# Performance work log

Measured on AMD Instinct MI355X. Metric: run time of the kernel, lower is better.

## Reference

```python
import jax, jax.numpy as jnp
import numpy as np

P = 16; IMG = 800; GRID = IMG // P; NP = GRID * GRID  # 2500 patches
D = P * P * 3  # 768
H = 8; HD = D // H; FF = 2048; L = 2; B = 2
NM = NP // 2; NV = NP - NM  # 1250 / 1250


def _ln(x, g, b):
    m = x.mean(-1, keepdims=True)
    v = ((x - m) ** 2).mean(-1, keepdims=True)
    return (x - m) * jax.lax.rsqrt(v + 1e-5) * g + b


def _block(x, qkv_w, qkv_b, out_w, out_b, w1, b1, w2, b2, g1, be1, g2, be2):
    # pre-LN-free MAE block: attn -> add&norm -> FFN -> add&norm (dropout in eval = identity)
    Bb, N, _ = x.shape
    qkv = (x @ qkv_w + qkv_b).reshape(Bb, N, 3, H, HD)
    q, k, v = qkv[:, :, 0], qkv[:, :, 1], qkv[:, :, 2]  # [B,N,H,HD]
    scores = jnp.einsum('bnhd,bmhd->bhnm', q, k) / np.float32(np.sqrt(HD))
    w = jax.nn.softmax(scores, axis=-1)
    ao = jnp.einsum('bhnm,bmhd->bnhd', w, v).reshape(Bb, N, D) @ out_w + out_b
    x = _ln(x + ao, g1, be1)
    f = jax.nn.relu(x @ w1 + b1) @ w2 + b2
    return _ln(x + f, g2, be2)


def _patchify(x):
    Bb = x.shape[0]
    # torch unfold(2,P,P).unfold(3,P,P) -> [B,C,h,w,p,p] -> [B,h*w,C*p*p]
    return x.reshape(Bb, 3, GRID, P, GRID, P).transpose(0, 2, 4, 1, 3, 5).reshape(Bb, NP, D)


def setup_inputs() -> dict:
    key = jax.random.key(0)
    ks = jax.random.split(key, 32)
    inp = {}
    inp['x'] = jax.random.normal(ks[0], (B, 3, IMG, IMG), jnp.float32)
    perm = jax.vmap(lambda k: jax.random.permutation(k, NP))(jax.random.split(ks[1], B))
    inp['visible_idx'] = perm[:, NM:].astype(jnp.int32)  # perm order, like torch
    inp['masked_idx'] = perm[:, :NM].astype(jnp.int32)
    c = [2]
    def nx(shape, s=0.02):
        k = ks[c[0]]; c[0] += 1
        return jax.random.normal(k, shape, jnp.float32) * s
    for p in ['enc', 'dec']:
        inp[p + '_qkv_w'] = nx((L, D, 3 * D)); inp[p + '_qkv_b'] = jnp.zeros((L, 3 * D), jnp.float32)
        inp[p + '_out_w'] = nx((L, D, D));     inp[p + '_out_b'] = jnp.zeros((L, D), jnp.float32)
        inp[p + '_w1'] = nx((L, D, FF));       inp[p + '_b1'] = jnp.zeros((L, FF), jnp.float32)
        inp[p + '_w2'] = nx((L, FF, D));       inp[p + '_b2'] = jnp.zeros((L, D), jnp.float32)
        inp[p + '_g1'] = jnp.ones((L, D), jnp.float32);  inp[p + '_be1'] = jnp.zeros((L, D), jnp.float32)
        inp[p + '_g2'] = jnp.ones((L, D), jnp.float32);  inp[p + '_be2'] = jnp.zeros((L, D), jnp.float32)
    inp['out_w'] = nx((D, D)); inp['out_b'] = jnp.zeros((D,), jnp.float32)
    inp['mask_token'] = nx((D,))
    inp['enc_pos'] = nx((NV, D))
    inp['dec_pos'] = nx((NP, D))
    return inp


def reference(x, visible_idx, masked_idx,
              enc_qkv_w, enc_qkv_b, enc_out_w, enc_out_b, enc_w1, enc_b1, enc_w2, enc_b2,
              enc_g1, enc_be1, enc_g2, enc_be2,
              dec_qkv_w, dec_qkv_b, dec_out_w, dec_out_b, dec_w1, dec_b1, dec_w2, dec_b2,
              dec_g1, dec_be1, dec_g2, dec_be2,
              out_w, out_b, mask_token, enc_pos, dec_pos):
    patches = _patchify(x)                                    # [B,NP,D]
    b_ix = jnp.arange(B)[:, None]
    vis = patches[b_ix, visible_idx]                          # [B,NV,D] in perm order
    h = vis + enc_pos[None]
    for i in range(L):
        h = _block(h, enc_qkv_w[i], enc_qkv_b[i], enc_out_w[i], enc_out_b[i],
                   enc_w1[i], enc_b1[i], enc_w2[i], enc_b2[i],
                   enc_g1[i], enc_be1[i], enc_g2[i], enc_be2[i])
    # torch: full_sequence[mask==0] = visible_patches (row-major positions <- perm-order rows)
    vis_pos = jnp.sort(visible_idx, axis=1)
    full = jnp.broadcast_to(mask_token, (B, NP, D))           # masked positions = mask_token
    full = full.at[b_ix, vis_pos].set(h)
    h = full + dec_pos[None]
    for i in range(L):
        h = _block(h, dec_qkv_w[i], dec_qkv_b[i], dec_out_w[i], dec_out_b[i],
                   dec_w1[i], dec_b1[i], dec_w2[i], dec_b2[i],
                   dec_g1[i], dec_be1[i], dec_g2[i], dec_be2[i])
    return h @ out_w + out_b                                  # [B,NP,D]
```

## Files before the change

kernel.cpp:

```cpp
#include <hip/hip_runtime.h>
#include <hip/hip_bf16.h>
#include <cstdint>
#include <cstddef>


#define NBATCH  2
#define NPATCH  2500
#define NVIS    1250
#define DMODEL  768
#define NHEAD   8
#define HDIM    96
#define FFDIM   2048
#define NPADV   2560

typedef __attribute__((ext_vector_type(8))) short bf16x8;
typedef __attribute__((ext_vector_type(4))) float f32x4;

__device__ __forceinline__ short f2bf(float f){
  union { float f; unsigned u; } x; x.f = f;
  unsigned r = x.u + 0x7fffu + ((x.u >> 16) & 1u);
  return (short)(r >> 16);
}

__device__ __forceinline__ void async_copy16(void* lds, const void* g){
  __builtin_amdgcn_global_load_lds(
      (const __attribute__((address_space(1))) unsigned int*)g,
      (__attribute__((address_space(3))) unsigned int*)lds, 16, 0, 0);
}

struct TJob { const float* src; short* dst; int K; int N; int tile_base; int tiles_x; };
struct TJobs { TJob j[17]; };

__global__ __launch_bounds__(256) void transpose_all_kernel(TJobs jobs){
  int bid = blockIdx.x;
  int ji = 0;
  #pragma unroll
  for (int k=1;k<17;k++) if (bid >= jobs.j[k].tile_base) ji = k;
  TJob jb = jobs.j[ji];
  int lt = bid - jb.tile_base;
  int tx = lt % jb.tiles_x, ty = lt / jb.tiles_x;
  __shared__ float tile[32][33];
  int lx = threadIdx.x & 31, ly = threadIdx.x >> 5;
  #pragma unroll
  for (int r=0;r<4;r++)
    tile[ly + r*8][lx] = jb.src[(size_t)(ty*32 + ly + r*8)*jb.N + tx*32 + lx];
  __syncthreads();
  #pragma unroll
  for (int r=0;r<4;r++)
    jb.dst[(size_t)(tx*32 + ly + r*8)*jb.K + ty*32 + lx] = f2bf(tile[lx][ly + r*8]);
}

template<int MODE>
__global__ __launch_bounds__(256) void gemm_kernel(const short* __restrict__ A,
    const short* __restrict__ Wt, const float* __restrict__ bias,
    short* __restrict__ Cb, float* __restrict__ Cf, int M, int Nc, int K){
  __shared__ short ldsA[128*64];
  __shared__ short ldsB[128*64];
  const int t = threadIdx.x, w = t>>6, ln = t&63;
  const int m0 = blockIdx.x*128, n0 = blockIdx.y*128;
  const int wr = (w>>1)*64, wc = (w&1)*64;
  const f32x4 fz = {0.f,0.f,0.f,0.f};
  f32x4 acc[4][4];
  #pragma unroll
  for (int mi=0;mi<4;mi++)
    #pragma unroll
    for (int ni=0;ni<4;ni++) acc[mi][ni] = fz;
  const int nkt = K >> 6;
  for (int kt=0; kt<nkt; kt++){
    #pragma unroll
    for (int c=0;c<4;c++){
      int chunk = c*256 + t;
      int row = chunk>>3, seg = chunk&7, sgs = seg ^ (row&7);
      int gm = m0 + row; if (gm >= M) gm = M-1;
      async_copy16((char*)ldsA + c*4096 + w*1024, A  + (size_t)gm*K      + kt*64 + sgs*8);
      async_copy16((char*)ldsB + c*4096 + w*1024, Wt + (size_t)(n0+row)*K + kt*64 + sgs*8);
    }
    __syncthreads();
    #pragma unroll
    for (int ks=0;ks<2;ks++){
      bf16x8 af[4], bfr[4];
      #pragma unroll
      for (int mi=0;mi<4;mi++){
        int r = wr + mi*16 + (ln&15);
        int d = ks*4 + (ln>>4);
        af[mi]  = *(const bf16x8*)((const char*)ldsA + r*128 + ((d^(r&7))*16));
        int cc = wc + mi*16 + (ln&15);
        bfr[mi] = *(const bf16x8*)((const char*)ldsB + cc*128 + ((d^(cc&7))*16));
      }
      #pragma unroll
      for (int mi=0;mi<4;mi++)
        #pragma unroll
        for (int ni=0;ni<4;ni++)
          acc[mi][ni] = __builtin_amdgcn_mfma_f32_16x16x32_bf16(af[mi], bfr[ni], acc[mi][ni], 0,0,0);
    }
    __syncthreads();
  }
  float bv[4];
  #pragma unroll
  for (int ni=0;ni<4;ni++) bv[ni] = bias[n0 + wc + ni*16 + (ln&15)];
  #pragma unroll
  for (int mi=0;mi<4;mi++){
    #pragma unroll
    for (int j=0;j<4;j++){
      int gr = m0 + wr + mi*16 + (ln>>4)*4 + j;
      if (gr < M){
        #pragma unroll
        for (int ni=0;ni<4;ni++){
          float v = acc[mi][ni][j] + bv[ni];
          if (MODE==2) v = fmaxf(v, 0.f);
          int gc = n0 + wc + ni*16 + (ln&15);
          if (MODE==1) Cf[(size_t)gr*Nc + gc] = v;
          else         Cb[(size_t)gr*Nc + gc] = f2bf(v);
        }
      }
    }
  }
}

__global__ __launch_bounds__(256) void vtrans_kernel(const short* __restrict__ qkv,
    short* __restrict__ vt, int N){
  int bh = blockIdx.z;
  int b = bh >> 3, h = bh & 7;
  int n0 = blockIdx.x*32, hd0 = blockIdx.y*32;
  __shared__ short tile[32][33];
  int lx = threadIdx.x & 31, ly = threadIdx.x >> 5;
  #pragma unroll
  for (int r=0;r<4;r++){
    int n = n0 + ly + r*8;
    short val = 0;
    if (n < N) val = qkv[(size_t)(b*N+n)*2304 + 1536 + h*96 + hd0 + lx];
    tile[ly+r*8][lx] = val;
  }
  __syncthreads();
  #pragma unroll
  for (int r=0;r<4;r++){
    int hd = hd0 + ly + r*8, n = n0 + lx;
    vt[(size_t)(bh*96 + hd)*NPADV + n] = tile[lx][ly+r*8];
  }
}

__global__ __launch_bounds__(256) void attn_kernel(const short* __restrict__ qkv,
    const short* __restrict__ vt, short* __restrict__ ao, int N, int NT){
  __shared__ short Ks[64*128];
  __shared__ short Vs[96*64];
  __shared__ short Ps[4*1024];
  const int t = threadIdx.x, w = t>>6, ln = t&63;
  const int col = ln & 15, hi = ln >> 4;
  const int bh = blockIdx.y, b = bh >> 3, h = bh & 7;
  const int q0 = blockIdx.x * 64;
  short* Pw = &Ps[w*1024];
  const float scale2 = 0.14724974f;

  bf16x8 qf[3];
  {
    int gq = q0 + w*16 + col; if (gq >= N) gq = N-1;
    const short* qrow = qkv + (size_t)(b*N+gq)*2304 + h*96;
    #pragma unroll
    for (int ks=0;ks<3;ks++)
      qf[ks] = *(const bf16x8*)(qrow + ks*32 + hi*8);
  }
  const f32x4 fz = {0.f,0.f,0.f,0.f};
  f32x4 o[6];
  #pragma unroll
  for (int g=0; g<6; g++) o[g] = fz;
  float mrun = -3e38f;
  float srun = 0.f;

  for (int kt=0; kt<NT; kt++){
    int n0 = kt*64;
    #pragma unroll
    for (int i=0;i<4;i++){
      int chunk = i*256 + t, row = chunk>>4, seg = chunk&15;
      int s2 = seg ^ (row&7);
      int gn = n0 + row; if (gn >= N) gn = N-1;
      const short* src = qkv + (size_t)(b*N+gn)*2304 + 768 + h*96
                       + ((s2 < 12) ? s2*8 : 0);
      async_copy16((char*)Ks + i*4096 + w*1024, src);
    }
    #pragma unroll
    for (int i=0;i<3;i++){
      int chunk = i*256 + t, row = chunk>>3, seg = chunk&7;
      int s2 = seg ^ (row&7);
      const short* src = vt + (size_t)(bh*96 + row)*NPADV + n0 + s2*8;
      async_copy16((char*)Vs + i*4096 + w*1024, src);
    }
    __syncthreads();

    f32x4 s[4];
    __builtin_amdgcn_s_setprio(1);
    #pragma unroll
    for (int tt=0;tt<4;tt++){
      f32x4 sc = fz;
      #pragma unroll
      for (int ks=0;ks<3;ks++){
        int r = tt*16 + col, d = ks*4 + hi;
        bf16x8 kb = *(const bf16x8*)((const char*)Ks + r*256 + ((d ^ (r&7))*16));
        sc = __builtin_amdgcn_mfma_f32_16x16x32_bf16(kb, qf[ks], sc, 0,0,0);
      }
      s[tt] = sc;
    }
    __builtin_amdgcn_s_setprio(0);

    if (n0 + 64 > N){
      #pragma unroll
      for (int tt=0;tt<4;tt++)
        #pragma unroll
        for (int j=0;j<4;j++)
          if (n0 + tt*16 + hi*4 + j >= N) s[tt][j] = -3e38f;
    }
    float mraw = s[0][0];
    #pragma unroll
    for (int tt=0;tt<4;tt++)
      #pragma unroll
      for (int j=0;j<4;j++) if (tt|j) mraw = fmaxf(mraw, s[tt][j]);
    mraw = fmaxf(mraw, __shfl_xor(mraw, 16));
    mraw = fmaxf(mraw, __shfl_xor(mraw, 32));
    float mxs = mraw * scale2;
    if (__any(mxs > mrun + 11.5f)){
      float mnew = fmaxf(mrun, mxs);
      float alpha = exp2f(mrun - mnew);
      mrun = mnew; srun *= alpha;
      float a0 = __shfl(alpha, hi*4+0), a1 = __shfl(alpha, hi*4+1);
      float a2 = __shfl(alpha, hi*4+2), a3 = __shfl(alpha, hi*4+3);
      #pragma unroll
      for (int g=0; g<6; g++){
        o[g][0] *= a0; o[g][1] *= a1; o[g][2] *= a2; o[g][3] *= a3;
      }
    }
    float psum = 0.f;
    #pragma unroll
    for (int tt=0;tt<4;tt++){
      float p0 = exp2f(fmaf(s[tt][0], scale2, -mrun));
      float p1 = exp2f(fmaf(s[tt][1], scale2, -mrun));
      float p2 = exp2f(fmaf(s[tt][2], scale2, -mrun));
      float p3 = exp2f(fmaf(s[tt][3], scale2, -mrun));
      psum += (p0+p1) + (p2+p3);
      __hip_bfloat162 lo = __float22bfloat162_rn(float2{p0,p1});
      __hip_bfloat162 hn = __float22bfloat162_rn(float2{p2,p3});
      uint2 pk; pk.x = *reinterpret_cast<unsigned*>(&lo);
      pk.y = *reinterpret_cast<unsigned*>(&hn);
      char* wp = (char*)Pw + col*128 + (((2*tt + (hi>>1)) ^ (col&7))<<4) + ((hi&1)<<3);
      *reinterpret_cast<uint2*>(wp) = pk;
    }
    srun += psum;
    __builtin_amdgcn_s_setprio(1);
    #pragma unroll
    for (int ks2=0; ks2<2; ks2++){
      bf16x8 pa = *(const bf16x8*)((const char*)Pw + col*128
                    + (((ks2*4 + hi) ^ (col&7))<<4));
      #pragma unroll
      for (int g=0; g<6; g++){
        int r = g*16 + col, d = ks2*4 + hi;
        bf16x8 vb = *(const bf16x8*)((const char*)Vs + r*128 + ((d ^ (r&7))*16));
        o[g] = __builtin_amdgcn_mfma_f32_16x16x32_bf16(pa, vb, o[g], 0,0,0);
      }
    }
    __builtin_amdgcn_s_setprio(0);
    __syncthreads();
  }
  srun += __shfl_xor(srun, 16);
  srun += __shfl_xor(srun, 32);
  float inv = 1.f / srun;
  float i0 = __shfl(inv, hi*4+0), i1 = __shfl(inv, hi*4+1);
  float i2 = __shfl(inv, hi*4+2), i3 = __shfl(inv, hi*4+3);
  #pragma unroll
  for (int g=0; g<6; g++){
    float ov[4] = {o[g][0]*i0, o[g][1]*i1, o[g][2]*i2, o[g][3]*i3};
    #pragma unroll
    for (int j=0;j<4;j++){
      int qr = q0 + w*16 + hi*4 + j;
      if (qr < N)
        ao[(size_t)(b*N+qr)*768 + h*96 + g*16 + col] = f2bf(ov[j]);
    }
  }
}

__global__ __launch_bounds__(256) void ln_kernel(const float* __restrict__ xin,
    const float* __restrict__ add, const float* __restrict__ g,
    const float* __restrict__ be, float* __restrict__ xo, short* __restrict__ xob){
  int row = blockIdx.x, t = threadIdx.x;
  float e[3]; float s = 0.f;
  #pragma unroll
  for (int k=0;k<3;k++){
    size_t off = (size_t)row*768 + t + k*256;
    e[k] = xin[off] + add[off]; s += e[k];
  }
  #pragma unroll
  for (int d=32; d; d>>=1) s += __shfl_xor(s, d);
  __shared__ float red[8];
  if ((t&63)==0) red[t>>6] = s;
  __syncthreads();
  float mean = (red[0]+red[1]+red[2]+red[3]) * (1.f/768.f);
  float vs = 0.f;
  #pragma unroll
  for (int k=0;k<3;k++){ float dd = e[k]-mean; vs += dd*dd; }
  #pragma unroll
  for (int d=32; d; d>>=1) vs += __shfl_xor(vs, d);
  if ((t&63)==0) red[4 + (t>>6)] = vs;
  __syncthreads();
  float rstd = rsqrtf((red[4]+red[5]+red[6]+red[7]) * (1.f/768.f) + 1e-5f);
  #pragma unroll
  for (int k=0;k<3;k++){
    int c = t + k*256;
    size_t off = (size_t)row*768 + c;
    float ov = (e[k]-mean)*rstd*g[c] + be[c];
    xo[off] = ov; xob[off] = f2bf(ov);
  }
}

__global__ __launch_bounds__(256) void patchify_kernel(const float* __restrict__ x,
    const int* __restrict__ vis, const float* __restrict__ enc_pos,
    float* __restrict__ xe, short* __restrict__ xeb){
  int b = blockIdx.y, i = blockIdx.x;
  int pidx = vis[b*NVIS + i];
  int gy = pidx / 50, gx = pidx - gy*50;
  #pragma unroll
  for (int k=0;k<3;k++){
    int d = threadIdx.x + k*256;
    int c = d >> 8, rr = d & 255, py = rr >> 4, px = rr & 15;
    float v = x[(((size_t)b*3 + c)*800 + gy*16 + py)*800 + gx*16 + px]
            + enc_pos[(size_t)i*768 + d];
    size_t off = (size_t)(b*NVIS + i)*768 + d;
    xe[off] = v; xeb[off] = f2bf(v);
  }
}

__global__ __launch_bounds__(256) void rank_kernel(const int* __restrict__ vis,
    int* __restrict__ rnk){
  int b = blockIdx.y; int i = blockIdx.x*256 + threadIdx.x;
  if (i >= NVIS) return;
  int p = vis[b*NVIS + i]; int c = 0;
  for (int j=0;j<NVIS;j++) c += (vis[b*NVIS + j] < p) ? 1 : 0;
  rnk[b*NVIS + i] = c;
}

__global__ __launch_bounds__(256) void dec_init_kernel(const float* __restrict__ mask_token,
    const float* __restrict__ dec_pos, float* __restrict__ xd, short* __restrict__ xdb){
  int row = blockIdx.x;
  int p = row % NPATCH;
  #pragma unroll
  for (int k=0;k<3;k++){
    int c = threadIdx.x + k*256;
    float v = mask_token[c] + dec_pos[(size_t)p*768 + c];
    size_t off = (size_t)row*768 + c;
    xd[off] = v; xdb[off] = f2bf(v);
  }
}

__global__ __launch_bounds__(256) void scatter_kernel(const int* __restrict__ vis,
    const int* __restrict__ rnk, const float* __restrict__ xe,
    const float* __restrict__ dec_pos, float* __restrict__ xd, short* __restrict__ xdb){
  int b = blockIdx.y, i = blockIdx.x;
  int p = vis[b*NVIS+i]; int r = rnk[b*NVIS+i];
  #pragma unroll
  for (int k=0;k<3;k++){
    int c = threadIdx.x + k*256;
    float v = xe[(size_t)(b*NVIS + r)*768 + c] + dec_pos[(size_t)p*768 + c];
    size_t off = (size_t)(b*NPATCH + p)*768 + c;
    xd[off] = v; xdb[off] = f2bf(v);
  }
}

static void run_block(hipStream_t stream, float* xf, short* xb, int M, int N, int NT,
                      const short* wqkvT, const float* qkv_b, const short* woutT,
                      const float* out_b, const short* w1T, const float* b1,
                      const short* w2T, const float* b2,
                      const float* g1, const float* be1, const float* g2, const float* be2,
                      short* qkvb, short* vt, short* aob, short* ffnb, float* tmp){
  int mt = (M + 127)/128;
  gemm_kernel<0><<<dim3(mt, 18), 256, 0, stream>>>(xb, wqkvT, qkv_b, qkvb, nullptr, M, 2304, 768);
  vtrans_kernel<<<dim3(NT*2, 3, 16), 256, 0, stream>>>(qkvb, vt, N);
  attn_kernel<<<dim3(NT, 16), 256, 0, stream>>>(qkvb, vt, aob, N, NT);
  gemm_kernel<1><<<dim3(mt, 6), 256, 0, stream>>>(aob, woutT, out_b, nullptr, tmp, M, 768, 768);
  ln_kernel<<<M, 256, 0, stream>>>(xf, tmp, g1, be1, xf, xb);
  gemm_kernel<2><<<dim3(mt, 16), 256, 0, stream>>>(xb, w1T, b1, ffnb, nullptr, M, 2048, 768);
  gemm_kernel<1><<<dim3(mt, 6), 256, 0, stream>>>(ffnb, w2T, b2, nullptr, tmp, M, 768, 2048);
  ln_kernel<<<M, 256, 0, stream>>>(xf, tmp, g2, be2, xf, xb);
}

extern "C" void kernel_launch(void* const* d_in, const int* in_sizes, int n_in,
                              void* d_out, int out_size, void* d_ws, size_t ws_size,
                              hipStream_t stream){
  const float* x        = (const float*)d_in[0];
  const int*   vis      = (const int*)d_in[1];
  const float* eqkv_w   = (const float*)d_in[3];
  const float* eqkv_b   = (const float*)d_in[4];
  const float* eout_w   = (const float*)d_in[5];
  const float* eout_b   = (const float*)d_in[6];
  const float* ew1      = (const float*)d_in[7];
  const float* eb1      = (const float*)d_in[8];
  const float* ew2      = (const float*)d_in[9];
  const float* eb2      = (const float*)d_in[10];
  const float* eg1      = (const float*)d_in[11];
  const float* ebe1     = (const float*)d_in[12];
  const float* eg2      = (const float*)d_in[13];
  const float* ebe2     = (const float*)d_in[14];
  const float* dqkv_w   = (const float*)d_in[15];
  const float* dqkv_b   = (const float*)d_in[16];
  const float* dout_w   = (const float*)d_in[17];
  const float* dout_b   = (const float*)d_in[18];
  const float* dw1      = (const float*)d_in[19];
  const float* db1      = (const float*)d_in[20];
  const float* dw2      = (const float*)d_in[21];
  const float* db2      = (const float*)d_in[22];
  const float* dg1      = (const float*)d_in[23];
  const float* dbe1     = (const float*)d_in[24];
  const float* dg2      = (const float*)d_in[25];
  const float* dbe2     = (const float*)d_in[26];
  const float* fout_w   = (const float*)d_in[27];
  const float* fout_b   = (const float*)d_in[28];
  const float* mask_tok = (const float*)d_in[29];
  const float* enc_posp = (const float*)d_in[30];
  const float* dec_posp = (const float*)d_in[31];

  char* p = (char*)d_ws;
  auto alloc = [&](size_t bytes)->char*{ char* r = p; p += (bytes + 255) & ~(size_t)255; return r; };

  const float* qkvw_s[2] = {eqkv_w, dqkv_w};
  const float* outw_s[2] = {eout_w, dout_w};
  const float* w1_s[2]   = {ew1, dw1};
  const float* w2_s[2]   = {ew2, dw2};

  short *wq[2][2], *wo[2][2], *w1t[2][2], *w2t[2][2];
  TJobs jobs; int jidx = 0; int tbase = 0;
  auto addJob = [&](const float* src, short* dst, int K, int N){
    jobs.j[jidx].src = src; jobs.j[jidx].dst = dst; jobs.j[jidx].K = K; jobs.j[jidx].N = N;
    jobs.j[jidx].tile_base = tbase; jobs.j[jidx].tiles_x = N/32;
    tbase += (K/32)*(N/32); jidx++;
  };
  for (int s=0;s<2;s++)
    for (int i=0;i<2;i++){
      wq[s][i]  = (short*)alloc((size_t)2304*768*2);
      addJob(qkvw_s[s] + (size_t)i*768*2304, wq[s][i], 768, 2304);
      wo[s][i]  = (short*)alloc((size_t)768*768*2);
      addJob(outw_s[s] + (size_t)i*768*768, wo[s][i], 768, 768);
      w1t[s][i] = (short*)alloc((size_t)2048*768*2);
      addJob(w1_s[s] + (size_t)i*768*2048, w1t[s][i], 768, 2048);
      w2t[s][i] = (short*)alloc((size_t)768*2048*2);
      addJob(w2_s[s] + (size_t)i*2048*768, w2t[s][i], 2048, 768);
    }
  short* wfin = (short*)alloc((size_t)768*768*2);
  addJob(fout_w, wfin, 768, 768);
  int total_tiles = tbase;

  float* xe   = (float*)alloc((size_t)2500*768*4);
  short* xeb  = (short*)alloc((size_t)2500*768*2);
  float* xd   = (float*)alloc((size_t)5000*768*4);
  short* xdb  = (short*)alloc((size_t)5000*768*2);
  short* qkvb = (short*)alloc((size_t)5000*2304*2);
  short* vt   = (short*)alloc((size_t)16*96*NPADV*2);
  short* aob  = (short*)alloc((size_t)5000*768*2);
  short* ffnb = (short*)alloc((size_t)5000*2048*2);
  float* tmp  = (float*)alloc((size_t)5000*768*4);
  int*   rnk  = (int*)alloc((size_t)2*NVIS*4);

  transpose_all_kernel<<<total_tiles, 256, 0, stream>>>(jobs);
  patchify_kernel<<<dim3(NVIS, NBATCH), 256, 0, stream>>>(x, vis, enc_posp, xe, xeb);
  rank_kernel<<<dim3((NVIS+255)/256, NBATCH), 256, 0, stream>>>(vis, rnk);

  for (int i=0;i<2;i++)
    run_block(stream, xe, xeb, 2500, 1250, 20,
              wq[0][i], eqkv_b + i*2304, wo[0][i], eout_b + i*768,
              w1t[0][i], eb1 + i*2048, w2t[0][i], eb2 + i*768,
              eg1 + i*768, ebe1 + i*768, eg2 + i*768, ebe2 + i*768,
              qkvb, vt, aob, ffnb, tmp);

  dec_init_kernel<<<NBATCH*NPATCH, 256, 0, stream>>>(mask_tok, dec_posp, xd, xdb);
  scatter_kernel<<<dim3(NVIS, NBATCH), 256, 0, stream>>>(vis, rnk, xe, dec_posp, xd, xdb);

  for (int i=0;i<2;i++)
    run_block(stream, xd, xdb, 5000, 2500, 40,
              wq[1][i], dqkv_b + i*2304, wo[1][i], dout_b + i*768,
              w1t[1][i], db1 + i*2048, w2t[1][i], db2 + i*768,
              dg1 + i*768, dbe1 + i*768, dg2 + i*768, dbe2 + i*768,
              qkvb, vt, aob, ffnb, tmp);

  gemm_kernel<1><<<dim3(40, 6), 256, 0, stream>>>(xdb, wfin, fout_b, nullptr,
                                                  (float*)d_out, 5000, 768, 768);
}
```

Measured before the change: 1.022 ms.

## Split KV range in attention and split-K the narrow-output GEMMs

```diff
diff --git a/kernel.cpp b/kernel.cpp
--- a/kernel.cpp
+++ b/kernel.cpp
@@ -53,11 +53,13 @@
 template<int MODE>
 __global__ __launch_bounds__(256) void gemm_kernel(const short* __restrict__ A,
     const short* __restrict__ Wt, const float* __restrict__ bias,
-    short* __restrict__ Cb, float* __restrict__ Cf, int M, int Nc, int K){
+    short* __restrict__ Cb, float* __restrict__ Cf0, float* __restrict__ Cf1,
+    int M, int Nc, int K, int nkt_per){
   __shared__ short ldsA[128*64];
   __shared__ short ldsB[128*64];
   const int t = threadIdx.x, w = t>>6, ln = t&63;
   const int m0 = blockIdx.x*128, n0 = blockIdx.y*128;
+  const int z = blockIdx.z;
   const int wr = (w>>1)*64, wc = (w&1)*64;
   const f32x4 fz = {0.f,0.f,0.f,0.f};
   f32x4 acc[4][4];
@@ -65,8 +67,9 @@
   for (int mi=0;mi<4;mi++)
     #pragma unroll
     for (int ni=0;ni<4;ni++) acc[mi][ni] = fz;
-  const int nkt = K >> 6;
-  for (int kt=0; kt<nkt; kt++){
+  const int ktb = z*nkt_per;
+  for (int kk=0; kk<nkt_per; kk++){
+    int kt = ktb + kk;
     #pragma unroll
     for (int c=0;c<4;c++){
       int chunk = c*256 + t;
@@ -97,7 +100,9 @@
   }
   float bv[4];
   #pragma unroll
-  for (int ni=0;ni<4;ni++) bv[ni] = bias[n0 + wc + ni*16 + (ln&15)];
+  for (int ni=0;ni<4;ni++)
+    bv[ni] = (z==0) ? bias[n0 + wc + ni*16 + (ln&15)] : 0.f;
+  float* Cf = (z==0) ? Cf0 : Cf1;
   #pragma unroll
   for (int mi=0;mi<4;mi++){
     #pragma unroll
@@ -140,7 +145,8 @@
 }
 
 __global__ __launch_bounds__(256) void attn_kernel(const short* __restrict__ qkv,
-    const short* __restrict__ vt, short* __restrict__ ao, int N, int NT){
+    const short* __restrict__ vt, float* __restrict__ poA, float* __restrict__ poB,
+    float* __restrict__ pm, float* __restrict__ pl, int N, int NT, int TPS, int half){
   __shared__ short Ks[64*128];
   __shared__ short Vs[96*64];
   __shared__ short Ps[4*1024];
@@ -148,6 +154,8 @@
   const int col = ln & 15, hi = ln >> 4;
   const int bh = blockIdx.y, b = bh >> 3, h = bh & 7;
   const int q0 = blockIdx.x * 64;
+  const int z = blockIdx.z;
+  const int kt0 = z*TPS, kt1 = (kt0 + TPS < NT) ? kt0 + TPS : NT;
   short* Pw = &Ps[w*1024];
   const float scale2 = 0.14724974f;
 
@@ -166,7 +174,7 @@
   float mrun = -3e38f;
   float srun = 0.f;
 
-  for (int kt=0; kt<NT; kt++){
+  for (int kt=kt0; kt<kt1; kt++){
     int n0 = kt*64;
     #pragma unroll
     for (int i=0;i<4;i++){
@@ -260,30 +268,63 @@
   }
   srun += __shfl_xor(srun, 16);
   srun += __shfl_xor(srun, 32);
-  float inv = 1.f / srun;
-  float i0 = __shfl(inv, hi*4+0), i1 = __shfl(inv, hi*4+1);
-  float i2 = __shfl(inv, hi*4+2), i3 = __shfl(inv, hi*4+3);
-  #pragma unroll
-  for (int g=0; g<6; g++){
-    float ov[4] = {o[g][0]*i0, o[g][1]*i1, o[g][2]*i2, o[g][3]*i3};
+  int qrow = q0 + w*16 + col;
+  if (hi == 0 && qrow < N){
+    size_t mi = ((size_t)(z*2 + b)*8 + h)*2560 + qrow;
+    pm[mi] = mrun; pl[mi] = srun;
+  }
+  size_t spl = (size_t)2*N*768;
+  float* po = (z < half) ? (poA + (size_t)z*spl)
+                         : (poB + (size_t)(z-half)*spl);
+  #pragma unroll
+  for (int g=0; g<6; g++)
     #pragma unroll
     for (int j=0;j<4;j++){
       int qr = q0 + w*16 + hi*4 + j;
       if (qr < N)
-        ao[(size_t)(b*N+qr)*768 + h*96 + g*16 + col] = f2bf(ov[j]);
-    }
+        po[(size_t)(b*N+qr)*768 + h*96 + g*16 + col] = o[g][j];
+    }
+}
+
+__global__ __launch_bounds__(256) void attn_merge_kernel(const float* __restrict__ poA,
+    const float* __restrict__ poB, const float* __restrict__ pm,
+    const float* __restrict__ pl, short* __restrict__ ao, int N, int NS){
+  int x = blockIdx.x; int b = x / N, qr = x - b*N;
+  int t = threadIdx.x;
+  int half = NS >> 1;
+  size_t rowoff = (size_t)(b*N+qr)*768;
+  size_t spl = (size_t)2*N*768;
+  #pragma unroll
+  for (int k=0;k<3;k++){
+    int c = t + k*256;
+    int h = c/96;
+    size_t mi0 = ((size_t)b*8 + h)*2560 + qr;
+    float m = -3e38f;
+    for (int s=0;s<NS;s++)
+      m = fmaxf(m, pm[(size_t)s*(2*8*2560) + mi0]);
+    float num = 0.f, den = 0.f;
+    for (int s=0;s<NS;s++){
+      size_t base = (size_t)s*(2*8*2560) + mi0;
+      float wgt = exp2f(pm[base] - m);
+      den += pl[base]*wgt;
+      const float* po = (s < half) ? poA + (size_t)s*spl
+                                   : poB + (size_t)(s-half)*spl;
+      num += po[rowoff + c]*wgt;
+    }
+    ao[rowoff + c] = f2bf(num/den);
   }
 }
 
 __global__ __launch_bounds__(256) void ln_kernel(const float* __restrict__ xin,
-    const float* __restrict__ add, const float* __restrict__ g,
-    const float* __restrict__ be, float* __restrict__ xo, short* __restrict__ xob){
+    const float* __restrict__ add0, const float* __restrict__ add1,
+    const float* __restrict__ g, const float* __restrict__ be,
+    float* __restrict__ xo, short* __restrict__ xob){
   int row = blockIdx.x, t = threadIdx.x;
   float e[3]; float s = 0.f;
   #pragma unroll
   for (int k=0;k<3;k++){
     size_t off = (size_t)row*768 + t + k*256;
-    e[k] = xin[off] + add[off]; s += e[k];
+    e[k] = xin[off] + add0[off] + add1[off]; s += e[k];
   }
   #pragma unroll
   for (int d=32; d; d>>=1) s += __shfl_xor(s, d);
@@ -306,6 +347,12 @@
     float ov = (e[k]-mean)*rstd*g[c] + be[c];
     xo[off] = ov; xob[off] = f2bf(ov);
   }
+}
+
+__global__ __launch_bounds__(256) void add2_kernel(const float* __restrict__ a,
+    const float* __restrict__ b, float* __restrict__ out, int n){
+  for (int i = blockIdx.x*256 + threadIdx.x; i < n; i += gridDim.x*256)
+    out[i] = a[i] + b[i];
 }
 
 __global__ __launch_bounds__(256) void patchify_kernel(const float* __restrict__ x,
@@ -362,20 +409,32 @@
 }
 
 static void run_block(hipStream_t stream, float* xf, short* xb, int M, int N, int NT,
+                      int NS,
                       const short* wqkvT, const float* qkv_b, const short* woutT,
                       const float* out_b, const short* w1T, const float* b1,
                       const short* w2T, const float* b2,
                       const float* g1, const float* be1, const float* g2, const float* be2,
-                      short* qkvb, short* vt, short* aob, short* ffnb, float* tmp){
+                      short* qkvb, short* vt, short* aob, short* ffnb,
+                      float* tmp, float* tmp2, float* pmb, float* plb){
   int mt = (M + 127)/128;
-  gemm_kernel<0><<<dim3(mt, 18), 256, 0, stream>>>(xb, wqkvT, qkv_b, qkvb, nullptr, M, 2304, 768);
+  int mtq = (N + 63)/64;
+  int TPS = (NT + NS - 1)/NS;
+  float* poA = tmp;
+  float* poB = (float*)ffnb;
+  gemm_kernel<0><<<dim3(mt, 18, 1), 256, 0, stream>>>(xb, wqkvT, qkv_b, qkvb,
+                                                      nullptr, nullptr, M, 2304, 768, 12);
   vtrans_kernel<<<dim3(NT*2, 3, 16), 256, 0, stream>>>(qkvb, vt, N);
-  attn_kernel<<<dim3(NT, 16), 256, 0, stream>>>(qkvb, vt, aob, N, NT);
-  gemm_kernel<1><<<dim3(mt, 6), 256, 0, stream>>>(aob, woutT, out_b, nullptr, tmp, M, 768, 768);
-  ln_kernel<<<M, 256, 0, stream>>>(xf, tmp, g1, be1, xf, xb);
-  gemm_kernel<2><<<dim3(mt, 16), 256, 0, stream>>>(xb, w1T, b1, ffnb, nullptr, M, 2048, 768);
-  gemm_kernel<1><<<dim3(mt, 6), 256, 0, stream>>>(ffnb, w2T, b2, nullptr, tmp, M, 768, 2048);
-  ln_kernel<<<M, 256, 0, stream>>>(xf, tmp, g2, be2, xf, xb);
+  attn_kernel<<<dim3(mtq, 16, NS), 256, 0, stream>>>(qkvb, vt, poA, poB, pmb, plb,
+                                                     N, NT, TPS, NS/2);
+  attn_merge_kernel<<<2*N, 256, 0, stream>>>(poA, poB, pmb, plb, aob, N, NS);
+  gemm_kernel<1><<<dim3(mt, 6, 2), 256, 0, stream>>>(aob, woutT, out_b, nullptr,
+                                                     tmp, tmp2, M, 768, 768, 6);
+  ln_kernel<<<M, 256, 0, stream>>>(xf, tmp, tmp2, g1, be1, xf, xb);
+  gemm_kernel<2><<<dim3(mt, 16, 1), 256, 0, stream>>>(xb, w1T, b1, ffnb,
+                                                      nullptr, nullptr, M, 2048, 768, 12);
+  gemm_kernel<1><<<dim3(mt, 6, 2), 256, 0, stream>>>(ffnb, w2T, b2, nullptr,
+                                                     tmp, tmp2, M, 768, 2048, 16);
+  ln_kernel<<<M, 256, 0, stream>>>(xf, tmp, tmp2, g2, be2, xf, xb);
 }
 
 extern "C" void kernel_launch(void* const* d_in, const int* in_sizes, int n_in,
@@ -452,29 +511,33 @@
   short* aob  = (short*)alloc((size_t)5000*768*2);
   short* ffnb = (short*)alloc((size_t)5000*2048*2);
   float* tmp  = (float*)alloc((size_t)5000*768*4);
+  float* pmb  = (float*)alloc((size_t)4*2*8*2560*4);
+  float* plb  = (float*)alloc((size_t)4*2*8*2560*4);
   int*   rnk  = (int*)alloc((size_t)2*NVIS*4);
+  float* tmp2 = (float*)qkvb;
 
   transpose_all_kernel<<<total_tiles, 256, 0, stream>>>(jobs);
   patchify_kernel<<<dim3(NVIS, NBATCH), 256, 0, stream>>>(x, vis, enc_posp, xe, xeb);
   rank_kernel<<<dim3((NVIS+255)/256, NBATCH), 256, 0, stream>>>(vis, rnk);
 
   for (int i=0;i<2;i++)
-    run_block(stream, xe, xeb, 2500, 1250, 20,
+    run_block(stream, xe, xeb, 2500, 1250, 20, 4,
               wq[0][i], eqkv_b + i*2304, wo[0][i], eout_b + i*768,
               w1t[0][i], eb1 + i*2048, w2t[0][i], eb2 + i*768,
               eg1 + i*768, ebe1 + i*768, eg2 + i*768, ebe2 + i*768,
-              qkvb, vt, aob, ffnb, tmp);
+              qkvb, vt, aob, ffnb, tmp, tmp2, pmb, plb);
 
   dec_init_kernel<<<NBATCH*NPATCH, 256, 0, stream>>>(mask_tok, dec_posp, xd, xdb);
   scatter_kernel<<<dim3(NVIS, NBATCH), 256, 0, stream>>>(vis, rnk, xe, dec_posp, xd, xdb);
 
   for (int i=0;i<2;i++)
-    run_block(stream, xd, xdb, 5000, 2500, 40,
+    run_block(stream, xd, xdb, 5000, 2500, 40, 2,
               wq[1][i], dqkv_b + i*2304, wo[1][i], dout_b + i*768,
               w1t[1][i], db1 + i*2048, w2t[1][i], db2 + i*768,
               dg1 + i*768, dbe1 + i*768, dg2 + i*768, dbe2 + i*768,
-              qkvb, vt, aob, ffnb, tmp);
-
-  gemm_kernel<1><<<dim3(40, 6), 256, 0, stream>>>(xdb, wfin, fout_b, nullptr,
-                                                  (float*)d_out, 5000, 768, 768);
-}
+              qkvb, vt, aob, ffnb, tmp, tmp2, pmb, plb);
+
+  gemm_kernel<1><<<dim3(40, 6, 2), 256, 0, stream>>>(xdb, wfin, fout_b, nullptr,
+                                                     tmp, tmp2, 5000, 768, 768, 6);
+  add2_kernel<<<2048, 256, 0, stream>>>(tmp, tmp2, (float*)d_out, 5000*768);
+}
```

Result: faster. 996.2 us (-2.5%).
